# Performance work log

Measured on AMD Instinct MI355X. Metric: run time of the kernel, lower is better.

Reference implementation:

```python
import jax, jax.numpy as jnp
import numpy as np

N_HEAD = 16
HEAD_DIM = 64  # n_embd // n_head = 1024 // 16

def setup_inputs() -> dict:
    key = jax.random.key(0)
    k1, k2, k3 = jax.random.split(key, 3)
    B, T, C = 4, 2048, 1024
    x = jax.random.normal(k1, (B, T, C), dtype=jnp.float32)
    w_qkv = jax.random.normal(k2, (3 * C, C), dtype=jnp.float32) * (C ** -0.5)
    w_proj = jax.random.normal(k3, (C, C), dtype=jnp.float32) * (C ** -0.5)
    b_proj = jnp.zeros((C,), dtype=jnp.float32)
    return {"x": x, "w_qkv": w_qkv, "w_proj": w_proj, "b_proj": b_proj}

def reference(x, w_qkv, w_proj, b_proj):
    B, T, C = x.shape
    H, hd = N_HEAD, HEAD_DIM
    # fused QKV projection (no bias), torch Linear: x @ W^T
    qkv = jnp.einsum('btc,dc->btd', x, w_qkv)           # [B,T,3C]
    # module-specific reshape: per-head groups of 3*hd, then chunk into q,k,v
    qkv = qkv.reshape(B, T, H, 3 * hd)
    q, k, v = jnp.split(qkv, 3, axis=-1)                # each [B,T,H,hd]
    q = q.transpose(0, 2, 1, 3)                         # [B,H,T,hd]
    k = k.transpose(0, 2, 1, 3)
    v = v.transpose(0, 2, 1, 3)
    att = jnp.einsum('bhqd,bhkd->bhqk', q, k) * (hd ** -0.5)
    causal = jnp.tril(jnp.ones((T, T), dtype=bool))
    att = jnp.where(causal, att, -jnp.inf)
    att = jax.nn.softmax(att, axis=-1)
    out = jnp.einsum('bhqk,bhkd->bhqd', att, v)         # [B,H,T,hd]
    out = out.transpose(0, 2, 1, 3).reshape(B, T, C)
    out = jnp.einsum('btc,dc->btd', out, w_proj) + b_proj
    return out
```

## Files before the change

### kernel.cpp

```cpp
#include <hip/hip_runtime.h>
#include <hip/hip_bf16.h>

typedef __attribute__((ext_vector_type(8))) short bf16x8;
typedef __attribute__((ext_vector_type(4))) float f32x4;
typedef unsigned short u16;

__device__ __forceinline__ u16 f2bf(float f) {
    __hip_bfloat16 h = __float2bfloat16(f);
    return __builtin_bit_cast(u16, h);
}
__device__ __forceinline__ bf16x8 load8(const u16* p) {
    return *reinterpret_cast<const bf16x8*>(p);
}
__device__ __forceinline__ void gl2lds16(const u16* g, u16* l) {
    __builtin_amdgcn_global_load_lds(
        (const __attribute__((address_space(1))) void*)g,
        (__attribute__((address_space(3))) void*)l, 16, 0, 0);
}

template<int CTRL>
__device__ __forceinline__ float dpp_mov(float v) {
    int b = __builtin_bit_cast(int, v);
    return __builtin_bit_cast(float,
        __builtin_amdgcn_update_dpp(b, b, CTRL, 0xF, 0xF, false));
}
__device__ __forceinline__ float rsum16(float v) {
    v += dpp_mov<0x121>(v);
    v += dpp_mov<0x122>(v);
    v += dpp_mov<0x124>(v);
    v += dpp_mov<0x128>(v);
    return v;
}

#define QSCALE 0.1803368801111244f

__global__ __launch_bounds__(256) void cast_f32_bf16(
    const float* __restrict__ src, u16* __restrict__ dst, int n4)
{
    int i = blockIdx.x * blockDim.x + threadIdx.x;
    if (i < n4) {
        float4 f = reinterpret_cast<const float4*>(src)[i];
        ushort4 o;
        o.x = f2bf(f.x); o.y = f2bf(f.y); o.z = f2bf(f.z); o.w = f2bf(f.w);
        reinterpret_cast<ushort4*>(dst)[i] = o;
    }
}

#define GEMM128_BODY(EPILOGUE)                                                 \
    __shared__ __align__(16) u16 As[128 * 32];                                 \
    __shared__ __align__(16) u16 Bs[128 * 32];                                 \
    const int t = threadIdx.x;                                                 \
    const int lane = t & 63;                                                   \
    const int wave = t >> 6;                                                   \
    const int quad = lane >> 4;                                                \
    const int lid  = lane & 15;                                                \
    const int wrow = wave & 1;                                                 \
    const int wcol = wave >> 1;                                                \
    const int mtile = blockIdx.x * 128;                                        \
    const int ntile = blockIdx.y * 128;                                        \
    const int srow = t >> 2;                                                   \
    const int scol = (t & 3) * 8;                                              \
    const u16* ga0 = Aptr + (size_t)(mtile + srow) * 1024 + scol;              \
    const u16* ga1 = Aptr + (size_t)(mtile + 64 + srow) * 1024 + scol;         \
    const u16* gb0 = Bptr + (size_t)(ntile + srow) * 1024 + scol;              \
    const u16* gb1 = Bptr + (size_t)(ntile + 64 + srow) * 1024 + scol;         \
    u16* la0 = As + t * 8;                                                     \
    u16* la1 = As + (256 + t) * 8;                                             \
    u16* lb0 = Bs + t * 8;                                                     \
    u16* lb1 = Bs + (256 + t) * 8;                                             \
    f32x4 acc[4][4] = {};                                                      \
    const int aro = wrow * 64 * 32 + quad * 8;                                 \
    const int bro = wcol * 64 * 32 + quad * 8;                                 \
    for (int k0 = 0; k0 < 1024; k0 += 32) {                                    \
        __syncthreads();                                                       \
        gl2lds16(ga0 + k0, la0);                                               \
        gl2lds16(ga1 + k0, la1);                                               \
        gl2lds16(gb0 + k0, lb0);                                               \
        gl2lds16(gb1 + k0, lb1);                                               \
        __syncthreads();                                                       \
        bf16x8 a[4], b[4];                                                     \
        _Pragma("unroll")                                                      \
        for (int i = 0; i < 4; ++i) {                                          \
            a[i] = load8(As + aro + (i * 16 + lid) * 32);                      \
            b[i] = load8(Bs + bro + (i * 16 + lid) * 32);                      \
        }                                                                      \
        _Pragma("unroll")                                                      \
        for (int mi = 0; mi < 4; ++mi)                                         \
            _Pragma("unroll")                                                  \
            for (int ni = 0; ni < 4; ++ni)                                     \
                acc[mi][ni] = __builtin_amdgcn_mfma_f32_16x16x32_bf16(         \
                    a[mi], b[ni], acc[mi][ni], 0, 0, 0);                       \
    }                                                                          \
    EPILOGUE

__global__ __launch_bounds__(256) void qkv_gemm128(
    const u16* __restrict__ Aptr, const u16* __restrict__ Bptr,
    u16* __restrict__ Q, u16* __restrict__ K, u16* __restrict__ Vt)
{
    GEMM128_BODY(
    _Pragma("unroll")
    for (int mi = 0; mi < 4; ++mi)
        _Pragma("unroll")
        for (int ni = 0; ni < 4; ++ni)
            _Pragma("unroll")
            for (int r = 0; r < 4; ++r) {
                int m = mtile + wrow * 64 + mi * 16 + quad * 4 + r;
                int n = ntile + wcol * 64 + ni * 16 + lid;
                int h = n / 192;
                int rr = n - h * 192;
                int sel = rr >> 6;
                int d = rr & 63;
                float v = acc[mi][ni][r];
                if (sel == 2)
                    Vt[((size_t)h * 64 + d) * 8192 + m] = f2bf(v);
                else if (sel == 0)
                    Q[((size_t)h * 8192 + m) * 64 + d] = f2bf(v * QSCALE);
                else
                    K[((size_t)h * 8192 + m) * 64 + d] = f2bf(v);
            }
    )
}

__global__ __launch_bounds__(256) void proj_gemm128(
    const u16* __restrict__ Aptr, const u16* __restrict__ Bptr,
    const float* __restrict__ bias, float* __restrict__ out)
{
    GEMM128_BODY(
    _Pragma("unroll")
    for (int mi = 0; mi < 4; ++mi)
        _Pragma("unroll")
        for (int ni = 0; ni < 4; ++ni)
            _Pragma("unroll")
            for (int r = 0; r < 4; ++r) {
                int m = mtile + wrow * 64 + mi * 16 + quad * 4 + r;
                int n = ntile + wcol * 64 + ni * 16 + lid;
                out[(size_t)m * 1024 + n] = acc[mi][ni][r] + bias[n];
            }
    )
}

__global__ __launch_bounds__(256) void attn(
    const u16* __restrict__ Q, const u16* __restrict__ K,
    const u16* __restrict__ Vtg, u16* __restrict__ O)
{
    const int qt = 31 - (blockIdx.x >> 6);
    const int bh = blockIdx.x & 63;
    const int b = bh >> 4, h = bh & 15;
    const int tid = threadIdx.x;
    const int lane = tid & 63;
    const int wave = tid >> 6;
    const int quad = lane >> 4;
    const int lid  = lane & 15;

    const size_t hb = ((size_t)h * 8192 + (size_t)b * 2048) * 64;
    const u16* Qp = Q + hb;
    const u16* Kp = K + hb;
    const u16* Vp = Vtg + (size_t)h * 64 * 8192 + (size_t)b * 2048;

    __shared__ __align__(16) u16 Vt[2][64 * 64];
    __shared__ __align__(16) u16 Ps[4][16][72];

    const int vd = tid >> 3, vslot = tid & 7;
    const int vchunk = vslot ^ (vd & 7);
    const u16* vg0 = Vp + (size_t)vd * 8192 + vchunk * 8;
    const u16* vg1 = vg0 + (size_t)32 * 8192;

    const int qbase = qt * 64;
    const int qw = qbase + wave * 16;
    const int qrow = qw + lid;

    bf16x8 aq0 = load8(Qp + (size_t)qrow * 64 + quad * 8);
    bf16x8 aq1 = load8(Qp + (size_t)qrow * 64 + 32 + quad * 8);

    f32x4 oacc[4] = {};
    float lacc[4] = {0.f, 0.f, 0.f, 0.f};

    const int nkt = qt + 1;

    gl2lds16(vg0, Vt[0] + tid * 8);
    gl2lds16(vg1, Vt[0] + 2048 + tid * 8);

    for (int kt = 0; kt < nkt; ++kt) {
        const int k0 = kt * 64;
        u16* vbuf = Vt[kt & 1];

        f32x4 s[4];
        __builtin_amdgcn_s_setprio(1);
#pragma unroll
        for (int nt = 0; nt < 4; ++nt) {
            const u16* kp = Kp + (size_t)(k0 + nt * 16 + lid) * 64 + quad * 8;
            f32x4 a = {0, 0, 0, 0};
            a = __builtin_amdgcn_mfma_f32_16x16x32_bf16(aq0, load8(kp), a, 0, 0, 0);
            a = __builtin_amdgcn_mfma_f32_16x16x32_bf16(aq1, load8(kp + 32), a, 0, 0, 0);
            s[nt] = a;
        }
        __builtin_amdgcn_s_setprio(0);

        const bool needmask = (k0 + 63 > qw);
#pragma unroll
        for (int r = 0; r < 4; ++r) {
            const int q = qw + quad * 4 + r;
            float p[4];
#pragma unroll
            for (int nt = 0; nt < 4; ++nt) {
                float sv = s[nt][r];
                if (needmask && (k0 + nt * 16 + lid > q)) sv = -1e30f;
                p[nt] = exp2f(sv);
                Ps[wave][quad * 4 + r][nt * 16 + lid] = f2bf(p[nt]);
            }
            lacc[r] += (p[0] + p[1]) + (p[2] + p[3]);
        }

        __syncthreads();

        if (kt + 1 < nkt) {
            const int kn = k0 + 64;
            u16* vnext = Vt[(kt + 1) & 1];
            gl2lds16(vg0 + kn, vnext + tid * 8);
            gl2lds16(vg1 + kn, vnext + 2048 + tid * 8);
        }

        bf16x8 ap0 = load8(&Ps[wave][lid][quad * 8]);
        bf16x8 ap1 = load8(&Ps[wave][lid][32 + quad * 8]);
        __builtin_amdgcn_s_setprio(1);
#pragma unroll
        for (int j = 0; j < 4; ++j) {
            const int row = j * 16 + lid;
            const int s0 = quad ^ (lid & 7);
            const int s1 = (4 + quad) ^ (lid & 7);
            bf16x8 bv0 = load8(vbuf + row * 64 + s0 * 8);
            bf16x8 bv1 = load8(vbuf + row * 64 + s1 * 8);
            oacc[j] = __builtin_amdgcn_mfma_f32_16x16x32_bf16(ap0, bv0, oacc[j], 0, 0, 0);
            oacc[j] = __builtin_amdgcn_mfma_f32_16x16x32_bf16(ap1, bv1, oacc[j], 0, 0, 0);
        }
        __builtin_amdgcn_s_setprio(0);
    }

    float inv_l[4];
#pragma unroll
    for (int r = 0; r < 4; ++r) inv_l[r] = 1.0f / rsum16(lacc[r]);
#pragma unroll
    for (int j = 0; j < 4; ++j)
#pragma unroll
        for (int r = 0; r < 4; ++r) {
            int ml = qbase + wave * 16 + quad * 4 + r;
            int col = h * 64 + j * 16 + lid;
            O[(size_t)(b * 2048 + ml) * 1024 + col] = f2bf(oacc[j][r] * inv_l[r]);
        }
}

extern "C" void kernel_launch(void* const* d_in, const int* in_sizes, int n_in,
                              void* d_out, int out_size, void* d_ws, size_t ws_size,
                              hipStream_t stream) {
    const float* x      = (const float*)d_in[0];
    const float* w_qkv  = (const float*)d_in[1];
    const float* w_proj = (const float*)d_in[2];
    const float* b_proj = (const float*)d_in[3];
    float* out = (float*)d_out;

    u16* Q   = (u16*)d_ws;
    u16* K   = Q   + (size_t)16 * 8192 * 64;
    u16* Vt  = K   + (size_t)16 * 8192 * 64;
    u16* A2  = Vt  + (size_t)16 * 64 * 8192;
    u16* Xb  = A2  + (size_t)8192 * 1024;
    u16* Wqb = Xb  + (size_t)8192 * 1024;
    u16* Wpb = Wqb + (size_t)3072 * 1024;

    cast_f32_bf16<<<dim3(8192), 256, 0, stream>>>(x, Xb, 8192 * 1024 / 4);
    cast_f32_bf16<<<dim3(3072), 256, 0, stream>>>(w_qkv, Wqb, 3072 * 1024 / 4);
    cast_f32_bf16<<<dim3(1024), 256, 0, stream>>>(w_proj, Wpb, 1024 * 1024 / 4);

    qkv_gemm128<<<dim3(64, 24), 256, 0, stream>>>(Xb, Wqb, Q, K, Vt);
    attn<<<dim3(2048), 256, 0, stream>>>(Q, K, Vt, A2);
    proj_gemm128<<<dim3(64, 8), 256, 0, stream>>>(A2, Wpb, b_proj, out);
}
```

Before: 333.0 us.

## Rewrite attention with 32x32 MFMA, 128-row query tiles and register-resident P

The attention kernel now computes S transposed (K·Q) with 32x32x16 bf16 MFMAs, so each wave owns 32 query rows and a block covers 128 queries. Grid size halves and each V tile in LDS is reused across more queries. P is packed to bf16 in registers via v_cvt_pk_bf16_f32 and a cross-half lane shuffle, so the LDS round-trip for P goes away. Waves whose causal range ends early skip compute but still join the barriers, and the 16-lane DPP row-sum reduction becomes a single shuffle. The larger per-wave accumulators raise register pressure, and the launch bounds request four blocks per CU.

```diff
diff --git a/kernel.cpp b/kernel.cpp
--- a/kernel.cpp
+++ b/kernel.cpp
@@ -3,6 +3,8 @@
 
 typedef __attribute__((ext_vector_type(8))) short bf16x8;
 typedef __attribute__((ext_vector_type(4))) float f32x4;
+typedef __attribute__((ext_vector_type(16))) float f32x16;
+typedef __attribute__((ext_vector_type(4))) int i32x4;
 typedef unsigned short u16;
 
 __device__ __forceinline__ u16 f2bf(float f) {
@@ -17,19 +19,10 @@
         (const __attribute__((address_space(1))) void*)g,
         (__attribute__((address_space(3))) void*)l, 16, 0, 0);
 }
-
-template<int CTRL>
-__device__ __forceinline__ float dpp_mov(float v) {
-    int b = __builtin_bit_cast(int, v);
-    return __builtin_bit_cast(float,
-        __builtin_amdgcn_update_dpp(b, b, CTRL, 0xF, 0xF, false));
-}
-__device__ __forceinline__ float rsum16(float v) {
-    v += dpp_mov<0x121>(v);
-    v += dpp_mov<0x122>(v);
-    v += dpp_mov<0x124>(v);
-    v += dpp_mov<0x128>(v);
-    return v;
+__device__ __forceinline__ unsigned int cvtpk(float lo, float hi) {
+    unsigned int r;
+    asm("v_cvt_pk_bf16_f32 %0, %1, %2" : "=v"(r) : "v"(lo), "v"(hi));
+    return r;
 }
 
 #define QSCALE 0.1803368801111244f
@@ -139,18 +132,18 @@
     )
 }
 
-__global__ __launch_bounds__(256) void attn(
+__global__ __launch_bounds__(256, 4) void attn(
     const u16* __restrict__ Q, const u16* __restrict__ K,
     const u16* __restrict__ Vtg, u16* __restrict__ O)
 {
-    const int qt = 31 - (blockIdx.x >> 6);
+    const int qtile = 15 - (blockIdx.x >> 6);
     const int bh = blockIdx.x & 63;
     const int b = bh >> 4, h = bh & 15;
     const int tid = threadIdx.x;
     const int lane = tid & 63;
     const int wave = tid >> 6;
-    const int quad = lane >> 4;
-    const int lid  = lane & 15;
+    const int c31 = lane & 31;
+    const int ht  = lane >> 5;
 
     const size_t hb = ((size_t)h * 8192 + (size_t)b * 2048) * 64;
     const u16* Qp = Q + hb;
@@ -158,57 +151,87 @@
     const u16* Vp = Vtg + (size_t)h * 64 * 8192 + (size_t)b * 2048;
 
     __shared__ __align__(16) u16 Vt[2][64 * 64];
-    __shared__ __align__(16) u16 Ps[4][16][72];
 
     const int vd = tid >> 3, vslot = tid & 7;
     const int vchunk = vslot ^ (vd & 7);
     const u16* vg0 = Vp + (size_t)vd * 8192 + vchunk * 8;
     const u16* vg1 = vg0 + (size_t)32 * 8192;
 
-    const int qbase = qt * 64;
-    const int qw = qbase + wave * 16;
-    const int qrow = qw + lid;
-
-    bf16x8 aq0 = load8(Qp + (size_t)qrow * 64 + quad * 8);
-    bf16x8 aq1 = load8(Qp + (size_t)qrow * 64 + 32 + quad * 8);
-
-    f32x4 oacc[4] = {};
-    float lacc[4] = {0.f, 0.f, 0.f, 0.f};
-
-    const int nkt = qt + 1;
+    const int qb = qtile * 128;
+    const int qw = qb + wave * 32;
+    const int q  = qw + c31;
+
+    bf16x8 qf[4];
+#pragma unroll
+    for (int dm = 0; dm < 4; ++dm)
+        qf[dm] = load8(Qp + (size_t)q * 64 + dm * 16 + ht * 8);
+
+    f32x16 od0 = {}, od1 = {};
+    float lsum = 0.f;
+
+    const int nkt   = 2 * qtile + 2;
+    const int nkt_w = 2 * qtile + ((wave < 2) ? 1 : 2);
 
     gl2lds16(vg0, Vt[0] + tid * 8);
     gl2lds16(vg1, Vt[0] + 2048 + tid * 8);
+
+#define SOFTMAX_KB(ST, KBOFF, PF0, PF1)                                        \
+    {                                                                          \
+        float pv[16];                                                          \
+        _Pragma("unroll")                                                      \
+        for (int r = 0; r < 16; ++r) {                                         \
+            const int kg = k0 + (KBOFF) + (r & 3) + 8 * (r >> 2) + 4 * ht;     \
+            float sv = ST[r];                                                  \
+            if (needmask && kg > q) sv = -1e30f;                               \
+            const float p = exp2f(sv);                                         \
+            pv[r] = p;                                                         \
+            lsum += p;                                                         \
+        }                                                                      \
+        _Pragma("unroll")                                                      \
+        for (int a = 0; a < 2; ++a) {                                          \
+            unsigned int u  = cvtpk(pv[8 * a + 0], pv[8 * a + 1]);             \
+            unsigned int u2 = cvtpk(pv[8 * a + 2], pv[8 * a + 3]);             \
+            unsigned int v  = cvtpk(pv[8 * a + 4], pv[8 * a + 5]);             \
+            unsigned int v2 = cvtpk(pv[8 * a + 6], pv[8 * a + 7]);             \
+            int r1 = __shfl_xor((int)(ht ? u : v), 32, 64);                    \
+            int r2 = __shfl_xor((int)(ht ? u2 : v2), 32, 64);                  \
+            i32x4 w;                                                           \
+            w.x = ht ? r1 : (int)u;                                            \
+            w.y = ht ? r2 : (int)u2;                                           \
+            w.z = ht ? (int)v : r1;                                            \
+            w.w = ht ? (int)v2 : r2;                                           \
+            ((a) ? (PF1) : (PF0)) = __builtin_bit_cast(bf16x8, w);             \
+        }                                                                      \
+    }
 
     for (int kt = 0; kt < nkt; ++kt) {
         const int k0 = kt * 64;
         u16* vbuf = Vt[kt & 1];
-
-        f32x4 s[4];
-        __builtin_amdgcn_s_setprio(1);
-#pragma unroll
-        for (int nt = 0; nt < 4; ++nt) {
-            const u16* kp = Kp + (size_t)(k0 + nt * 16 + lid) * 64 + quad * 8;
-            f32x4 a = {0, 0, 0, 0};
-            a = __builtin_amdgcn_mfma_f32_16x16x32_bf16(aq0, load8(kp), a, 0, 0, 0);
-            a = __builtin_amdgcn_mfma_f32_16x16x32_bf16(aq1, load8(kp + 32), a, 0, 0, 0);
-            s[nt] = a;
-        }
-        __builtin_amdgcn_s_setprio(0);
-
-        const bool needmask = (k0 + 63 > qw);
-#pragma unroll
-        for (int r = 0; r < 4; ++r) {
-            const int q = qw + quad * 4 + r;
-            float p[4];
-#pragma unroll
-            for (int nt = 0; nt < 4; ++nt) {
-                float sv = s[nt][r];
-                if (needmask && (k0 + nt * 16 + lid > q)) sv = -1e30f;
-                p[nt] = exp2f(sv);
-                Ps[wave][quad * 4 + r][nt * 16 + lid] = f2bf(p[nt]);
-            }
-            lacc[r] += (p[0] + p[1]) + (p[2] + p[3]);
+        const bool active = kt < nkt_w;
+        bf16x8 pf[4];
+
+        if (active) {
+            const bool needmask = (k0 + 63 > qw);
+            bf16x8 kfA[4], kfB[4];
+#pragma unroll
+            for (int dm = 0; dm < 4; ++dm)
+                kfA[dm] = load8(Kp + (size_t)(k0 + c31) * 64 + dm * 16 + ht * 8);
+#pragma unroll
+            for (int dm = 0; dm < 4; ++dm)
+                kfB[dm] = load8(Kp + (size_t)(k0 + 32 + c31) * 64 + dm * 16 + ht * 8);
+
+            f32x16 stA = {}, stB = {};
+            __builtin_amdgcn_s_setprio(1);
+#pragma unroll
+            for (int dm = 0; dm < 4; ++dm)
+                stA = __builtin_amdgcn_mfma_f32_32x32x16_bf16(kfA[dm], qf[dm], stA, 0, 0, 0);
+#pragma unroll
+            for (int dm = 0; dm < 4; ++dm)
+                stB = __builtin_amdgcn_mfma_f32_32x32x16_bf16(kfB[dm], qf[dm], stB, 0, 0, 0);
+            __builtin_amdgcn_s_setprio(0);
+
+            SOFTMAX_KB(stA, 0,  pf[0], pf[1]);
+            SOFTMAX_KB(stB, 32, pf[2], pf[3]);
         }
 
         __syncthreads();
@@ -220,33 +243,37 @@
             gl2lds16(vg1 + kn, vnext + 2048 + tid * 8);
         }
 
-        bf16x8 ap0 = load8(&Ps[wave][lid][quad * 8]);
-        bf16x8 ap1 = load8(&Ps[wave][lid][32 + quad * 8]);
-        __builtin_amdgcn_s_setprio(1);
-#pragma unroll
-        for (int j = 0; j < 4; ++j) {
-            const int row = j * 16 + lid;
-            const int s0 = quad ^ (lid & 7);
-            const int s1 = (4 + quad) ^ (lid & 7);
-            bf16x8 bv0 = load8(vbuf + row * 64 + s0 * 8);
-            bf16x8 bv1 = load8(vbuf + row * 64 + s1 * 8);
-            oacc[j] = __builtin_amdgcn_mfma_f32_16x16x32_bf16(ap0, bv0, oacc[j], 0, 0, 0);
-            oacc[j] = __builtin_amdgcn_mfma_f32_16x16x32_bf16(ap1, bv1, oacc[j], 0, 0, 0);
+        if (active) {
+            __builtin_amdgcn_s_setprio(1);
+#pragma unroll
+            for (int km = 0; km < 4; ++km) {
+                const int sl = ((km * 2 + ht) ^ (c31 & 7)) * 8;
+                bf16x8 v0 = load8(vbuf + c31 * 64 + sl);
+                bf16x8 v1 = load8(vbuf + (32 + c31) * 64 + sl);
+                od0 = __builtin_amdgcn_mfma_f32_32x32x16_bf16(v0, pf[km], od0, 0, 0, 0);
+                od1 = __builtin_amdgcn_mfma_f32_32x32x16_bf16(v1, pf[km], od1, 0, 0, 0);
+            }
+            __builtin_amdgcn_s_setprio(0);
         }
-        __builtin_amdgcn_s_setprio(0);
     }
 
-    float inv_l[4];
-#pragma unroll
-    for (int r = 0; r < 4; ++r) inv_l[r] = 1.0f / rsum16(lacc[r]);
-#pragma unroll
-    for (int j = 0; j < 4; ++j)
-#pragma unroll
-        for (int r = 0; r < 4; ++r) {
-            int ml = qbase + wave * 16 + quad * 4 + r;
-            int col = h * 64 + j * 16 + lid;
-            O[(size_t)(b * 2048 + ml) * 1024 + col] = f2bf(oacc[j][r] * inv_l[r]);
-        }
+    const float tot = lsum +
+        __builtin_bit_cast(float, __shfl_xor(__builtin_bit_cast(int, lsum), 32, 64));
+    const float inv = 1.0f / tot;
+
+    const size_t orow = (size_t)(b * 2048 + q) * 1024 + h * 64;
+#pragma unroll
+    for (int tp = 0; tp < 8; ++tp) {
+        const int r = 2 * tp;
+        const int d = (r & 3) + 8 * (r >> 2) + 4 * ht;
+        unsigned int w0 = (unsigned int)f2bf(od0[r] * inv) |
+                          ((unsigned int)f2bf(od0[r + 1] * inv) << 16);
+        unsigned int w1 = (unsigned int)f2bf(od1[r] * inv) |
+                          ((unsigned int)f2bf(od1[r + 1] * inv) << 16);
+        *reinterpret_cast<unsigned int*>(const_cast<u16*>(O) + orow + d) = w0;
+        *reinterpret_cast<unsigned int*>(const_cast<u16*>(O) + orow + 32 + d) = w1;
+    }
+#undef SOFTMAX_KB
 }
 
 extern "C" void kernel_launch(void* const* d_in, const int* in_sizes, int n_in,
@@ -271,6 +298,6 @@
     cast_f32_bf16<<<dim3(1024), 256, 0, stream>>>(w_proj, Wpb, 1024 * 1024 / 4);
 
     qkv_gemm128<<<dim3(64, 24), 256, 0, stream>>>(Xb, Wqb, Q, K, Vt);
-    attn<<<dim3(2048), 256, 0, stream>>>(Q, K, Vt, A2);
+    attn<<<dim3(1024), 256, 0, stream>>>(Q, K, Vt, A2);
     proj_gemm128<<<dim3(64, 8), 256, 0, stream>>>(A2, Wpb, b_proj, out);
 }
```

New measurement: 295.9 us. -11.1%, faster.
